# Performance work log

Hardware: AMD Instinct MI355X
Metric: run time of the kernel (lower is better)

The kernel has to match this reference:

```python
import jax, jax.numpy as jnp
import numpy as np

OBS, PRED, NAG, FIN, FOUT, H, NH, FF, NL = 8, 4, 256, 2, 2, 128, 8, 2048, 6


def _lin(x, w, b):
    return x @ w.T + b


def _ln(x, g, b, e=1e-5):
    m = x.mean(-1, keepdims=True)
    v = x.var(-1, keepdims=True)
    return (x - m) / jnp.sqrt(v + e) * g + b


def setup_inputs():
    key = jax.random.key(0)
    ks = iter(jax.random.split(key, 64))

    def w(shape, fan_in):
        return jax.random.normal(next(ks), shape, jnp.float32) / np.float32(np.sqrt(fan_in))

    return dict(
        traj_in=jax.random.normal(next(ks), (OBS + PRED, NAG, FIN), jnp.float32),
        adj_in=jax.random.uniform(next(ks), (OBS, NAG, NAG), jnp.float32),
        eps=jax.random.normal(next(ks), (OBS * NAG, H), jnp.float32),
        pro1_w=w((H, FIN), FIN), pro1_b=jnp.zeros(H, jnp.float32),
        pro2_w=w((H, H), H), pro2_b=jnp.zeros(H, jnp.float32),
        mu_w=w((H, H), H), mu_b=jnp.zeros(H, jnp.float32),
        ls_w=w((H, H), H), ls_b=jnp.zeros(H, jnp.float32),
        gdl_w=w((H, H), H), gdl_b=jnp.zeros(H, jnp.float32),
        pro3_w=w((H, OBS), OBS), pro3_b=jnp.zeros(H, jnp.float32),
        pro4_w=w((OBS, H), H), pro4_b=jnp.zeros(OBS, jnp.float32),
        pro5_w=w((FOUT, H), H), pro5_b=jnp.zeros(FOUT, jnp.float32),
        t_qkv_w=w((NL, 3 * H, H), H), t_qkv_b=jnp.zeros((NL, 3 * H), jnp.float32),
        t_out_w=w((NL, H, H), H), t_out_b=jnp.zeros((NL, H), jnp.float32),
        t_ff1_w=w((NL, FF, H), H), t_ff1_b=jnp.zeros((NL, FF), jnp.float32),
        t_ff2_w=w((NL, H, FF), FF), t_ff2_b=jnp.zeros((NL, H), jnp.float32),
        t_ln1_g=jnp.ones((NL, H), jnp.float32), t_ln1_b=jnp.zeros((NL, H), jnp.float32),
        t_ln2_g=jnp.ones((NL, H), jnp.float32), t_ln2_b=jnp.zeros((NL, H), jnp.float32),
        iftrain=1,
    )


def reference(traj_in, adj_in, eps, pro1_w, pro1_b, pro2_w, pro2_b, mu_w, mu_b,
              ls_w, ls_b, gdl_w, gdl_b, pro3_w, pro3_b, pro4_w, pro4_b,
              pro5_w, pro5_b, t_qkv_w, t_qkv_b, t_out_w, t_out_b,
              t_ff1_w, t_ff1_b, t_ff2_w, t_ff2_b, t_ln1_g, t_ln1_b,
              t_ln2_g, t_ln2_b, iftrain):
    batch_in = traj_in[:OBS, :, :FIN]            # [T, N, Fin]
    tar_y = traj_in[OBS:, :, :FOUT]              # [PRED, N, Fout]

    # block-diagonal adjacency over time, min-max normalized
    A = jax.scipy.linalg.block_diag(*[adj_in[t] for t in range(OBS)])  # [TN, TN]
    ADJ = (A - A.min()) / (A.max() - A.min())

    # GCNConv normalization: add remaining self-loops (weight 1), symmetric D^-1/2 A D^-1/2
    d = jnp.diagonal(ADJ)
    A_sl = ADJ + jnp.diag(jnp.where(d == 0, 1.0, 0.0).astype(ADJ.dtype))
    deg = A_sl.sum(0)
    dis = jnp.where(deg > 0, 1.0 / jnp.sqrt(deg), 0.0)
    agg = (dis[:, None] * A_sl * dis[None, :]).T  # aggregate src(row)->tgt(col)

    enc = _lin(jax.nn.relu(_lin(batch_in, pro1_w, pro1_b)), pro2_w, pro2_b)
    enc = enc.reshape(-1, H)                     # [TN, H]

    # VGAE encode (two GCNConv heads) + reparametrize, PyG clamps logstd at 10
    mu = agg @ _lin(enc, mu_w, mu_b)
    logstd = jnp.minimum(agg @ _lin(enc, ls_w, ls_b), 10.0)
    Z = jnp.where(jnp.asarray(iftrain) > 0, mu + eps * jnp.exp(logstd), mu)
    kld = -0.5 * jnp.mean(jnp.sum(1.0 + 2.0 * logstd - mu ** 2 - jnp.exp(2.0 * logstd), axis=1))

    out = _lin(Z, gdl_w, gdl_b)
    logits = Z @ Z.T                             # [TN, TN]
    struct_loss = jnp.mean(jnp.maximum(logits, 0.0) - logits * ADJ
                           + jnp.log1p(jnp.exp(-jnp.abs(logits))))

    # transformer over agents: [N, H, T] -> pro3 -> [N(seq), H(batch), H(d)]
    x = _lin(out.reshape(OBS, NAG, H).transpose(1, 2, 0), pro3_w, pro3_b)
    dh = H // NH
    S, B = x.shape[0], x.shape[1]
    for l in range(NL):
        qkv = _lin(x, t_qkv_w[l], t_qkv_b[l])
        q, k, v = jnp.split(qkv, 3, axis=-1)
        q = q.reshape(S, B, NH, dh)
        k = k.reshape(S, B, NH, dh)
        v = v.reshape(S, B, NH, dh)
        sc = jnp.einsum('sbhd,tbhd->bhst', q, k) / np.float32(np.sqrt(dh))
        att = jax.nn.softmax(sc, axis=-1)
        o = jnp.einsum('bhst,tbhd->sbhd', att, v).reshape(S, B, H)
        x = _ln(x + _lin(o, t_out_w[l], t_out_b[l]), t_ln1_g[l], t_ln1_b[l])
        f = _lin(jax.nn.relu(_lin(x, t_ff1_w[l], t_ff1_b[l])), t_ff2_w[l], t_ff2_b[l])
        x = _ln(x + f, t_ln2_g[l], t_ln2_b[l])

    out = _lin(x, pro4_w, pro4_b).transpose(2, 0, 1)   # [T, N, H]
    tra = _lin(out, pro5_w, pro5_b)                    # [T, N, Fout]
    traj = tra[-PRED:]
    traj_loss = jnp.sqrt(jnp.sum((traj - tar_y) ** 2, axis=-1)).sum(axis=0).mean()
    loss = traj_loss + kld + struct_loss
    return traj, loss
```

## Files before the change

kernel.cpp:

```cpp
#include <hip/hip_runtime.h>
#include <math.h>


namespace {

constexpr int kOBS = 8, kNAG = 256, kH = 128;
constexpr int kGN = kOBS * kNAG;
constexpr int kROWS = kNAG * kH;

typedef __attribute__((ext_vector_type(8))) short bf16x8;
typedef __attribute__((ext_vector_type(4))) float f32x4;
typedef __attribute__((ext_vector_type(4))) unsigned short us4;

struct Scal {
  int    mn_bits;
  int    mx_bits;
  float  Amin;
  float  invr;
  float  c0;
  int    pad;
  double kld_sum;
  double struct_sum;
  double traj_sum;
};

__device__ inline float waveReduceSum(float v) {
#pragma unroll
  for (int off = 32; off; off >>= 1) v += __shfl_xor(v, off, 64);
  return v;
}

__device__ inline unsigned short f2bf(float f) {
  unsigned u = __float_as_uint(f);
  return (unsigned short)((u + 0x7fffu + ((u >> 16) & 1u)) >> 16);
}
__device__ inline float bf2f(unsigned short h) {
  return __uint_as_float((unsigned)h << 16);
}
__device__ inline void split4(float4 v, us4& h, us4& l) {
  h.x = f2bf(v.x); l.x = f2bf(v.x - bf2f(h.x));
  h.y = f2bf(v.y); l.y = f2bf(v.y - bf2f(h.y));
  h.z = f2bf(v.z); l.z = f2bf(v.z - bf2f(h.z));
  h.w = f2bf(v.w); l.w = f2bf(v.w - bf2f(h.w));
}

__device__ inline int swz4(int c)  { return c ^ ((c >> 3) & 7); }
__device__ inline int swz16(int c) { return c ^ ((c >> 4) & 7); }

#define GLL(g, s)                                             \
  __builtin_amdgcn_global_load_lds(                           \
      (const __attribute__((address_space(1))) void*)(g),     \
      (__attribute__((address_space(3))) void*)(s), 16, 0, 0)

__global__ void k_init(Scal* sc) {
  if (threadIdx.x == 0) {
    sc->mn_bits = 0x7f800000;
    sc->mx_bits = 0xff800000;
    sc->kld_sum = 0.0;
    sc->struct_sum = 0.0;
    sc->traj_sum = 0.0;
  }
}

__global__ void k_minmax(const float* __restrict__ adj, int n, Scal* sc) {
  float lmin = INFINITY, lmax = -INFINITY;
  for (int i = blockIdx.x * blockDim.x + threadIdx.x; i < n;
       i += gridDim.x * blockDim.x) {
    float v = adj[i];
    lmin = fminf(lmin, v);
    lmax = fmaxf(lmax, v);
  }
#pragma unroll
  for (int off = 32; off; off >>= 1) {
    lmin = fminf(lmin, __shfl_xor(lmin, off, 64));
    lmax = fmaxf(lmax, __shfl_xor(lmax, off, 64));
  }
  __shared__ float smn[4], smx[4];
  int w = threadIdx.x >> 6;
  if ((threadIdx.x & 63) == 0) { smn[w] = lmin; smx[w] = lmax; }
  __syncthreads();
  if (threadIdx.x == 0) {
    lmin = fminf(fminf(smn[0], smn[1]), fminf(smn[2], smn[3]));
    lmax = fmaxf(fmaxf(smx[0], smx[1]), fmaxf(smx[2], smx[3]));
    atomicMin(&sc->mn_bits, __float_as_int(lmin));
    atomicMax(&sc->mx_bits, __float_as_int(lmax));
  }
}

__global__ void k_scale(Scal* sc) {
  float mn = fminf(0.0f, __int_as_float(sc->mn_bits));
  float mx = fmaxf(0.0f, __int_as_float(sc->mx_bits));
  sc->Amin = mn;
  sc->invr = 1.0f / (mx - mn);
  sc->c0 = (0.0f - mn) * sc->invr;
}

__global__ void k_dis(const float* __restrict__ adj, const Scal* __restrict__ sc,
                      float* __restrict__ dis) {
  int j = blockIdx.x * 256 + threadIdx.x;
  int t = j >> 8, jj = j & 255;
  const float* a = adj + (size_t)t * 65536;
  float Amin = sc->Amin, invr = sc->invr, c0 = sc->c0;
  float sum = 0.f;
  for (int i = 0; i < 256; ++i) sum += (a[i * 256 + jj] - Amin) * invr;
  float djj = (a[jj * 256 + jj] - Amin) * invr;
  float deg = sum + 1792.0f * c0 + (djj == 0.0f ? 1.0f : 0.0f);
  dis[j] = deg > 0.0f ? 1.0f / sqrtf(deg) : 0.0f;
}

__global__ void k_agg(const float* __restrict__ adj, const Scal* __restrict__ sc,
                      const float* __restrict__ dis, float* __restrict__ agg) {
  int idx = blockIdx.x * 256 + threadIdx.x;
  int t = idx >> 16, i = (idx >> 8) & 255, j = idx & 255;
  float v = (adj[(size_t)t * 65536 + j * 256 + i] - sc->Amin) * sc->invr;
  if (i == j && v == 0.0f) v += 1.0f;
  agg[idx] = dis[t * 256 + j] * v * dis[t * 256 + i];
}

__global__ void k_enc1(const float* __restrict__ traj, const float* __restrict__ w,
                       const float* __restrict__ b, float* __restrict__ out) {
  int idx = blockIdx.x * 256 + threadIdx.x;
  int r = idx >> 7, f = idx & 127;
  float v = traj[r * 2] * w[f * 2] + traj[r * 2 + 1] * w[f * 2 + 1] + b[f];
  out[idx] = fmaxf(v, 0.0f);
}

__global__ void k_cvt(const float* __restrict__ src, unsigned short* __restrict__ h,
                      unsigned short* __restrict__ l, int n4) {
  int i = blockIdx.x * 256 + threadIdx.x;
  if (i >= n4) return;
  float4 v = reinterpret_cast<const float4*>(src)[i];
  us4 hh, ll;
  split4(v, hh, ll);
  reinterpret_cast<us4*>(h)[i] = hh;
  reinterpret_cast<us4*>(l)[i] = ll;
}

#define BM 64
#define BN 64
#define KC 32
#define LP 68

template <bool TB>
__global__ __launch_bounds__(256) void gemm_kernel(
    const float* __restrict__ A, const float* __restrict__ B,
    const float* __restrict__ bias, float* __restrict__ C, int K, int ldb,
    int ldc, int flags, size_t aStride, size_t bStride, size_t cStride) {
  if (blockIdx.z) {
    A += (size_t)blockIdx.z * aStride;
    B += (size_t)blockIdx.z * bStride;
    C += (size_t)blockIdx.z * cStride;
  }
  __shared__ float As[KC][LP];
  __shared__ float Bs[KC][LP];
  const int tid = threadIdx.x;
  const int tx = tid & 15, ty = tid >> 4;
  const int m0 = blockIdx.y * BM, n0 = blockIdx.x * BN;
  float acc[4][4] = {};
  for (int k0 = 0; k0 < K; k0 += KC) {
#pragma unroll
    for (int i = 0; i < 2; ++i) {
      int q = tid + i * 256;
      int row = q >> 3, kq = q & 7;
      float4 v = *reinterpret_cast<const float4*>(
          &A[(size_t)(m0 + row) * K + k0 + kq * 4]);
      As[kq * 4 + 0][row] = v.x;
      As[kq * 4 + 1][row] = v.y;
      As[kq * 4 + 2][row] = v.z;
      As[kq * 4 + 3][row] = v.w;
    }
    if (TB) {
#pragma unroll
      for (int i = 0; i < 2; ++i) {
        int q = tid + i * 256;
        int row = q >> 3, kq = q & 7;
        float4 v = *reinterpret_cast<const float4*>(
            &B[(size_t)(n0 + row) * ldb + k0 + kq * 4]);
        Bs[kq * 4 + 0][row] = v.x;
        Bs[kq * 4 + 1][row] = v.y;
        Bs[kq * 4 + 2][row] = v.z;
        Bs[kq * 4 + 3][row] = v.w;
      }
    } else {
#pragma unroll
      for (int i = 0; i < 2; ++i) {
        int q = tid + i * 256;
        int kr = q >> 4, nq = q & 15;
        float4 v = *reinterpret_cast<const float4*>(
            &B[(size_t)(k0 + kr) * ldb + n0 + nq * 4]);
        *reinterpret_cast<float4*>(&Bs[kr][nq * 4]) = v;
      }
    }
    __syncthreads();
#pragma unroll
    for (int kk = 0; kk < KC; ++kk) {
      float4 a4 = *reinterpret_cast<const float4*>(&As[kk][ty * 4]);
      float4 b4 = *reinterpret_cast<const float4*>(&Bs[kk][tx * 4]);
      float av[4] = {a4.x, a4.y, a4.z, a4.w};
      float bv[4] = {b4.x, b4.y, b4.z, b4.w};
#pragma unroll
      for (int i = 0; i < 4; ++i)
#pragma unroll
        for (int j = 0; j < 4; ++j) acc[i][j] += av[i] * bv[j];
    }
    __syncthreads();
  }
  float bv[4] = {0.f, 0.f, 0.f, 0.f};
  if (bias) {
    float4 b4 = *reinterpret_cast<const float4*>(&bias[n0 + tx * 4]);
    bv[0] = b4.x; bv[1] = b4.y; bv[2] = b4.z; bv[3] = b4.w;
  }
#pragma unroll
  for (int i = 0; i < 4; ++i) {
    float* cp = &C[(size_t)(m0 + ty * 4 + i) * ldc + n0 + tx * 4];
    float4 o;
    float ov[4];
#pragma unroll
    for (int j = 0; j < 4; ++j) ov[j] = acc[i][j] + bv[j];
    if (flags & 2) {
      float4 old = *reinterpret_cast<const float4*>(cp);
      ov[0] += old.x; ov[1] += old.y; ov[2] += old.z; ov[3] += old.w;
    }
    if (flags & 1) {
#pragma unroll
      for (int j = 0; j < 4; ++j) ov[j] = fmaxf(ov[j], 0.0f);
    }
    o.x = ov[0]; o.y = ov[1]; o.z = ov[2]; o.w = ov[3];
    *reinterpret_cast<float4*>(cp) = o;
  }
}

template <int BMb, int BNb>
__global__ __launch_bounds__(256) void gemm_bf(
    const unsigned short* __restrict__ Ah, const unsigned short* __restrict__ Al,
    const unsigned short* __restrict__ Bh, const unsigned short* __restrict__ Bl,
    const float* __restrict__ bias, float* __restrict__ C,
    int K, int lda, int ldb, int ldc, int flags) {
  constexpr int MI = BMb / 32, NI = BNb / 32;
  constexpr int WTM = BMb / 2, WTN = BNb / 2;
  __shared__ unsigned short sAh[BMb * 32], sAl[BMb * 32];
  __shared__ unsigned short sBh[BNb * 32], sBl[BNb * 32];
  const int tid = threadIdx.x, lane = tid & 63, w = tid >> 6;
  const int wr = w >> 1, wc = w & 1;
  const int m0 = blockIdx.y * BMb, n0 = blockIdx.x * BNb;
  f32x4 acc[MI][NI];
#pragma unroll
  for (int i = 0; i < MI; ++i)
#pragma unroll
    for (int j = 0; j < NI; ++j) acc[i][j] = (f32x4){0.f, 0.f, 0.f, 0.f};

  for (int k0 = 0; k0 < K; k0 += 32) {
#pragma unroll
    for (int i = 0; i < BMb / 64; ++i) {
      int c = tid + i * 256;
      int g = swz4(c);
      int row = g >> 2, c4 = g & 3;
      size_t ga = (size_t)(m0 + row) * lda + k0 + c4 * 8;
      GLL(&Ah[ga], &sAh[c * 8]);
      GLL(&Al[ga], &sAl[c * 8]);
    }
#pragma unroll
    for (int i = 0; i < BNb / 64; ++i) {
      int c = tid + i * 256;
      int g = swz4(c);
      int row = g >> 2, c4 = g & 3;
      size_t ga = (size_t)(n0 + row) * ldb + k0 + c4 * 8;
      GLL(&Bh[ga], &sBh[c * 8]);
      GLL(&Bl[ga], &sBl[c * 8]);
    }
    __syncthreads();
    bf16x8 bh[NI], bl[NI];
#pragma unroll
    for (int ni = 0; ni < NI; ++ni) {
      int p = swz4((wc * WTN + ni * 16 + (lane & 15)) * 4 + (lane >> 4));
      bh[ni] = *reinterpret_cast<const bf16x8*>(&sBh[p * 8]);
      bl[ni] = *reinterpret_cast<const bf16x8*>(&sBl[p * 8]);
    }
#pragma unroll
    for (int mi = 0; mi < MI; ++mi) {
      int p = swz4((wr * WTM + mi * 16 + (lane & 15)) * 4 + (lane >> 4));
      bf16x8 ah = *reinterpret_cast<const bf16x8*>(&sAh[p * 8]);
      bf16x8 al = *reinterpret_cast<const bf16x8*>(&sAl[p * 8]);
#pragma unroll
      for (int ni = 0; ni < NI; ++ni) {
        acc[mi][ni] = __builtin_amdgcn_mfma_f32_16x16x32_bf16(
            ah, bh[ni], acc[mi][ni], 0, 0, 0);
        acc[mi][ni] = __builtin_amdgcn_mfma_f32_16x16x32_bf16(
            ah, bl[ni], acc[mi][ni], 0, 0, 0);
        acc[mi][ni] = __builtin_amdgcn_mfma_f32_16x16x32_bf16(
            al, bh[ni], acc[mi][ni], 0, 0, 0);
      }
    }
    __syncthreads();
  }
  const int crow0 = m0 + wr * WTM + (lane >> 4) * 4;
  const int ccol0 = n0 + wc * WTN + (lane & 15);
#pragma unroll
  for (int ni = 0; ni < NI; ++ni) {
    int col = ccol0 + ni * 16;
    float bv = bias ? bias[col] : 0.f;
#pragma unroll
    for (int mi = 0; mi < MI; ++mi) {
#pragma unroll
      for (int r = 0; r < 4; ++r) {
        int row = crow0 + mi * 16 + r;
        float v = acc[mi][ni][r] + bv;
        if (flags & 2) v += C[(size_t)row * ldc + col];
        if (flags & 1) v = fmaxf(v, 0.0f);
        C[(size_t)row * ldc + col] = v;
      }
    }
  }
}

__global__ __launch_bounds__(256) void k_ffn(
    const unsigned short* __restrict__ Xh, const unsigned short* __restrict__ Xl,
    const unsigned short* __restrict__ W1h, const unsigned short* __restrict__ W1l,
    const float* __restrict__ b1,
    const unsigned short* __restrict__ W2h, const unsigned short* __restrict__ W2l,
    const float* __restrict__ b2, float* __restrict__ out) {
  __shared__ unsigned short sLds[40960];
  unsigned short* sPh = sLds + 32768;
  unsigned short* sPl = sLds + 34816;
  float* sB1 = reinterpret_cast<float*>(sLds + 36864);
  const int tid = threadIdx.x, lane = tid & 63, w = tid >> 6;
  const int wr = w >> 1, wc = w & 1;
  const int m0 = blockIdx.x * 64;

  auto stageW = [&](int buf, int f0) {
    unsigned short* d = sLds + buf * 16384;
#pragma unroll
    for (int i = 0; i < 2; ++i) {
      int c = tid + i * 256;
      {
        int g = swz16(c);
        size_t ga = (size_t)(f0 + (g >> 4)) * 128 + (g & 15) * 8;
        GLL(&W1h[ga], &d[c * 8]);
        GLL(&W1l[ga], &d[4096 + c * 8]);
      }
      {
        int g = swz4(c);
        size_t ga = (size_t)(g >> 2) * 2048 + f0 + (g & 3) * 8;
        GLL(&W2h[ga], &d[8192 + c * 8]);
        GLL(&W2l[ga], &d[12288 + c * 8]);
      }
    }
  };

  {
    unsigned short* sXh = sLds + 16384;
    unsigned short* sXl = sLds + 24576;
#pragma unroll
    for (int i = 0; i < 4; ++i) {
      int c = tid + i * 256;
      int g = swz16(c);
      size_t ga = (size_t)(m0 + (g >> 4)) * 128 + (g & 15) * 8;
      GLL(&Xh[ga], &sXh[c * 8]);
      GLL(&Xl[ga], &sXl[c * 8]);
    }
#pragma unroll
    for (int i = 0; i < 2; ++i) {
      int c = tid + i * 256;
      GLL(&b1[c * 4], &sB1[c * 4]);
    }
  }
  __builtin_amdgcn_sched_barrier(0);
  asm volatile("s_waitcnt vmcnt(0)");
  __builtin_amdgcn_sched_barrier(0);
  __builtin_amdgcn_s_barrier();
  stageW(0, 0);
  bf16x8 xah[4][2], xal[4][2];
  {
    unsigned short* sXh = sLds + 16384;
    unsigned short* sXl = sLds + 24576;
#pragma unroll
    for (int ks = 0; ks < 4; ++ks)
#pragma unroll
      for (int mi = 0; mi < 2; ++mi) {
        int row = wr * 32 + mi * 16 + (lane & 15);
        int p = swz16(row * 16 + ks * 4 + (lane >> 4));
        xah[ks][mi] = *reinterpret_cast<const bf16x8*>(&sXh[p * 8]);
        xal[ks][mi] = *reinterpret_cast<const bf16x8*>(&sXl[p * 8]);
      }
  }
  __builtin_amdgcn_sched_barrier(0);
  asm volatile("s_waitcnt lgkmcnt(0)");
  __builtin_amdgcn_sched_barrier(0);
  __builtin_amdgcn_s_barrier();

  f32x4 acc2[2][4];
#pragma unroll
  for (int i = 0; i < 2; ++i)
#pragma unroll
    for (int j = 0; j < 4; ++j) acc2[i][j] = (f32x4){0.f, 0.f, 0.f, 0.f};

  const int pcol = wc * 16 + (lane & 15);

  auto body = [&](int cur, int f0, bool hasNext) {
    unsigned short* bW1h = sLds + cur * 16384;
    unsigned short* bW1l = bW1h + 4096;
    unsigned short* bW2h = bW1h + 8192;
    unsigned short* bW2l = bW1h + 12288;
    if (hasNext) {
      stageW(cur ^ 1, f0 + 32);
      __builtin_amdgcn_sched_barrier(0);
      asm volatile("s_waitcnt vmcnt(8)");
    } else {
      __builtin_amdgcn_sched_barrier(0);
      asm volatile("s_waitcnt vmcnt(0)");
    }
    __builtin_amdgcn_sched_barrier(0);
    __builtin_amdgcn_s_barrier();
    f32x4 acc1[2];
    acc1[0] = (f32x4){0.f, 0.f, 0.f, 0.f};
    acc1[1] = (f32x4){0.f, 0.f, 0.f, 0.f};
#pragma unroll
    for (int ks = 0; ks < 4; ++ks) {
      int p = swz16((wc * 16 + (lane & 15)) * 16 + ks * 4 + (lane >> 4));
      bf16x8 bh = *reinterpret_cast<const bf16x8*>(&bW1h[p * 8]);
      bf16x8 bl = *reinterpret_cast<const bf16x8*>(&bW1l[p * 8]);
#pragma unroll
      for (int mi = 0; mi < 2; ++mi) {
        acc1[mi] = __builtin_amdgcn_mfma_f32_16x16x32_bf16(xah[ks][mi], bh,
                                                           acc1[mi], 0, 0, 0);
        acc1[mi] = __builtin_amdgcn_mfma_f32_16x16x32_bf16(xah[ks][mi], bl,
                                                           acc1[mi], 0, 0, 0);
        acc1[mi] = __builtin_amdgcn_mfma_f32_16x16x32_bf16(xal[ks][mi], bh,
                                                           acc1[mi], 0, 0, 0);
      }
    }
    float b1v = sB1[f0 + pcol];
#pragma unroll
    for (int mi = 0; mi < 2; ++mi)
#pragma unroll
      for (int r = 0; r < 4; ++r) {
        int prow = wr * 32 + mi * 16 + (lane >> 4) * 4 + r;
        float v = fmaxf(acc1[mi][r] + b1v, 0.0f);
        unsigned short h = f2bf(v);
        int p = swz4(prow * 4 + (pcol >> 3));
        sPh[p * 8 + (pcol & 7)] = h;
        sPl[p * 8 + (pcol & 7)] = f2bf(v - bf2f(h));
      }
    __builtin_amdgcn_sched_barrier(0);
    asm volatile("s_waitcnt lgkmcnt(0)");
    __builtin_amdgcn_sched_barrier(0);
    __builtin_amdgcn_s_barrier();
    bf16x8 pah[2], pal[2];
#pragma unroll
    for (int mi = 0; mi < 2; ++mi) {
      int p = swz4((wr * 32 + mi * 16 + (lane & 15)) * 4 + (lane >> 4));
      pah[mi] = *reinterpret_cast<const bf16x8*>(&sPh[p * 8]);
      pal[mi] = *reinterpret_cast<const bf16x8*>(&sPl[p * 8]);
    }
#pragma unroll
    for (int ni = 0; ni < 4; ++ni) {
      int p = swz4((wc * 64 + ni * 16 + (lane & 15)) * 4 + (lane >> 4));
      bf16x8 bh = *reinterpret_cast<const bf16x8*>(&bW2h[p * 8]);
      bf16x8 bl = *reinterpret_cast<const bf16x8*>(&bW2l[p * 8]);
#pragma unroll
      for (int mi = 0; mi < 2; ++mi) {
        acc2[mi][ni] = __builtin_amdgcn_mfma_f32_16x16x32_bf16(
            pah[mi], bh, acc2[mi][ni], 0, 0, 0);
        acc2[mi][ni] = __builtin_amdgcn_mfma_f32_16x16x32_bf16(
            pah[mi], bl, acc2[mi][ni], 0, 0, 0);
        acc2[mi][ni] = __builtin_amdgcn_mfma_f32_16x16x32_bf16(
            pal[mi], bh, acc2[mi][ni], 0, 0, 0);
      }
    }
    __builtin_amdgcn_sched_barrier(0);
    __builtin_amdgcn_s_barrier();
  };

  for (int fc2 = 0; fc2 < 32; ++fc2) {
    body(0, fc2 * 64, true);
    body(1, fc2 * 64 + 32, fc2 != 31);
  }

#pragma unroll
  for (int ni = 0; ni < 4; ++ni) {
    int col = wc * 64 + ni * 16 + (lane & 15);
    float bv = b2[col];
#pragma unroll
    for (int mi = 0; mi < 2; ++mi)
#pragma unroll
      for (int r = 0; r < 4; ++r) {
        int row = m0 + wr * 32 + mi * 16 + (lane >> 4) * 4 + r;
        out[(size_t)row * 128 + col] = acc2[mi][ni][r] + bv;
      }
  }
}

__global__ void k_zkld(const float* __restrict__ mu, const float* __restrict__ lsr,
                       const float* __restrict__ eps, const int* __restrict__ iftrain,
                       float* __restrict__ Z, Scal* sc) {
  int i = blockIdx.x * 256 + threadIdx.x;
  float m = mu[i];
  float ls = fminf(lsr[i], 10.0f);
  float z = (*iftrain > 0) ? m + eps[i] * __expf(ls) : m;
  Z[i] = z;
  float kt = 1.0f + 2.0f * ls - m * m - __expf(2.0f * ls);
  kt = waveReduceSum(kt);
  __shared__ float sh[4];
  int w = threadIdx.x >> 6;
  if ((threadIdx.x & 63) == 0) sh[w] = kt;
  __syncthreads();
  if (threadIdx.x == 0)
    atomicAdd(&sc->kld_sum, (double)(sh[0] + sh[1] + sh[2] + sh[3]));
}

__global__ __launch_bounds__(256) void k_struct(const float* __restrict__ Z,
                                                const float* __restrict__ adj,
                                                Scal* sc) {
  __shared__ float As[KC][LP];
  __shared__ float Bs[KC][LP];
  const int tid = threadIdx.x;
  const int tx = tid & 15, ty = tid >> 4;
  const int m0 = blockIdx.y * BM, n0 = blockIdx.x * BN;
  float acc[4][4] = {};
  for (int k0 = 0; k0 < kH; k0 += KC) {
#pragma unroll
    for (int i = 0; i < 2; ++i) {
      int q = tid + i * 256;
      int row = q >> 3, kq = q & 7;
      float4 va = *reinterpret_cast<const float4*>(
          &Z[(size_t)(m0 + row) * kH + k0 + kq * 4]);
      As[kq * 4 + 0][row] = va.x;
      As[kq * 4 + 1][row] = va.y;
      As[kq * 4 + 2][row] = va.z;
      As[kq * 4 + 3][row] = va.w;
      float4 vb = *reinterpret_cast<const float4*>(
          &Z[(size_t)(n0 + row) * kH + k0 + kq * 4]);
      Bs[kq * 4 + 0][row] = vb.x;
      Bs[kq * 4 + 1][row] = vb.y;
      Bs[kq * 4 + 2][row] = vb.z;
      Bs[kq * 4 + 3][row] = vb.w;
    }
    __syncthreads();
#pragma unroll
    for (int kk = 0; kk < KC; ++kk) {
      float4 a4 = *reinterpret_cast<const float4*>(&As[kk][ty * 4]);
      float4 b4 = *reinterpret_cast<const float4*>(&Bs[kk][tx * 4]);
      float av[4] = {a4.x, a4.y, a4.z, a4.w};
      float bv[4] = {b4.x, b4.y, b4.z, b4.w};
#pragma unroll
      for (int i = 0; i < 4; ++i)
#pragma unroll
        for (int j = 0; j < 4; ++j) acc[i][j] += av[i] * bv[j];
    }
    __syncthreads();
  }
  float Amin = sc->Amin, invr = sc->invr, c0v = sc->c0;
  float lsum = 0.f;
#pragma unroll
  for (int i = 0; i < 4; ++i) {
#pragma unroll
    for (int j = 0; j < 4; ++j) {
      int gi = m0 + ty * 4 + i, gj = n0 + tx * 4 + j;
      float l = acc[i][j];
      float adjv = c0v;
      if ((gi >> 8) == (gj >> 8))
        adjv = (adj[((size_t)(gi >> 8) << 16) + (gi & 255) * 256 + (gj & 255)] -
                Amin) * invr;
      lsum += fmaxf(l, 0.0f) - l * adjv + __logf(1.0f + __expf(-fabsf(l)));
    }
  }
  lsum = waveReduceSum(lsum);
  __shared__ float sh[4];
  int w = threadIdx.x >> 6;
  if ((threadIdx.x & 63) == 0) sh[w] = lsum;
  __syncthreads();
  if (threadIdx.x == 0)
    atomicAdd(&sc->struct_sum, (double)(sh[0] + sh[1] + sh[2] + sh[3]));
}

__global__ void k_x0(const float* __restrict__ gdl, const float* __restrict__ w3,
                     const float* __restrict__ b3, float* __restrict__ X,
                     unsigned short* __restrict__ Xh,
                     unsigned short* __restrict__ Xl) {
  int f = threadIdx.x;
  size_t r = (size_t)blockIdx.x * 2 + threadIdx.y;
  int n = (int)(r >> 7), h = (int)(r & 127);
  float a = b3[f];
#pragma unroll
  for (int o = 0; o < 8; ++o)
    a += gdl[((size_t)o * 256 + n) * 128 + h] * w3[f * 8 + o];
  X[r * 128 + f] = a;
  unsigned short hh = f2bf(a);
  Xh[r * 128 + f] = hh;
  Xl[r * 128 + f] = f2bf(a - bf2f(hh));
}

__global__ __launch_bounds__(256) void k_attn(const float* __restrict__ QKV,
                                              unsigned short* __restrict__ Oh,
                                              unsigned short* __restrict__ Ol) {
  const int head = blockIdx.x, b = blockIdx.y;
  const int s = threadIdx.x;
  __shared__ float ks[256][16];
  __shared__ float vs[256][16];
  const size_t base = ((size_t)s * 128 + b) * 384 + head * 16;
#pragma unroll
  for (int i = 0; i < 4; ++i) {
    *reinterpret_cast<float4*>(&ks[s][i * 4]) =
        *reinterpret_cast<const float4*>(&QKV[base + 128 + i * 4]);
    *reinterpret_cast<float4*>(&vs[s][i * 4]) =
        *reinterpret_cast<const float4*>(&QKV[base + 256 + i * 4]);
  }
  float q[16];
#pragma unroll
  for (int i = 0; i < 4; ++i) {
    float4 v = *reinterpret_cast<const float4*>(&QKV[base + i * 4]);
    q[i * 4 + 0] = v.x * 0.25f; q[i * 4 + 1] = v.y * 0.25f;
    q[i * 4 + 2] = v.z * 0.25f; q[i * 4 + 3] = v.w * 0.25f;
  }
  __syncthreads();
  float m = -1e30f, lsum = 0.f;
  float o[16] = {};
#pragma unroll 2
  for (int t = 0; t < 256; ++t) {
    float kv[16], vv[16];
#pragma unroll
    for (int i = 0; i < 4; ++i) {
      float4 k4 = *reinterpret_cast<const float4*>(&ks[t][i * 4]);
      float4 v4 = *reinterpret_cast<const float4*>(&vs[t][i * 4]);
      kv[i * 4 + 0] = k4.x; kv[i * 4 + 1] = k4.y;
      kv[i * 4 + 2] = k4.z; kv[i * 4 + 3] = k4.w;
      vv[i * 4 + 0] = v4.x; vv[i * 4 + 1] = v4.y;
      vv[i * 4 + 2] = v4.z; vv[i * 4 + 3] = v4.w;
    }
    float d = 0.f;
#pragma unroll
    for (int i = 0; i < 16; ++i) d += q[i] * kv[i];
    if (d > m + 8.f) {
      float c = __expf(m - d);
      lsum *= c;
#pragma unroll
      for (int i = 0; i < 16; ++i) o[i] *= c;
      m = d;
    }
    float p = __expf(d - m);
    lsum += p;
#pragma unroll
    for (int i = 0; i < 16; ++i) o[i] += p * vv[i];
  }
  float inv = 1.0f / lsum;
  size_t ob = ((size_t)s * 128 + b) * 128 + head * 16;
#pragma unroll
  for (int i = 0; i < 4; ++i) {
    float4 v;
    v.x = o[i * 4 + 0] * inv; v.y = o[i * 4 + 1] * inv;
    v.z = o[i * 4 + 2] * inv; v.w = o[i * 4 + 3] * inv;
    us4 hh, ll;
    split4(v, hh, ll);
    *reinterpret_cast<us4*>(&Oh[ob + i * 4]) = hh;
    *reinterpret_cast<us4*>(&Ol[ob + i * 4]) = ll;
  }
}

__global__ __launch_bounds__(256) void k_resid_ln(
    float* __restrict__ X, const float* __restrict__ T,
    const float* __restrict__ g, const float* __restrict__ b,
    unsigned short* __restrict__ Xh, unsigned short* __restrict__ Xl) {
  int lane = threadIdx.x & 63, rl = threadIdx.x >> 6;
  size_t row = (size_t)blockIdx.x * 4 + rl;
  float* xp = X + row * 128;
  const float* tp = T + row * 128;
  float e0 = xp[lane] + tp[lane];
  float e1 = xp[lane + 64] + tp[lane + 64];
  float mean = waveReduceSum(e0 + e1) * 0.0078125f;
  float d0 = e0 - mean, d1 = e1 - mean;
  float var = waveReduceSum(d0 * d0 + d1 * d1) * 0.0078125f;
  float inv = 1.0f / sqrtf(var + 1e-5f);
  float v0 = d0 * inv * g[lane] + b[lane];
  float v1 = d1 * inv * g[lane + 64] + b[lane + 64];
  xp[lane] = v0;
  xp[lane + 64] = v1;
  unsigned short h0 = f2bf(v0), h1 = f2bf(v1);
  Xh[row * 128 + lane] = h0;
  Xl[row * 128 + lane] = f2bf(v0 - bf2f(h0));
  Xh[row * 128 + lane + 64] = h1;
  Xl[row * 128 + lane + 64] = f2bf(v1 - bf2f(h1));
}

__global__ void k_heady(const float* __restrict__ X, const float* __restrict__ w4,
                        const float* __restrict__ b4, float* __restrict__ y) {
  int tid = threadIdx.x;
  int o = tid & 7, rl = tid >> 3;
  size_t r = (size_t)blockIdx.x * 32 + rl;
  const float* xp = X + r * 128;
  const float* wp = w4 + o * 128;
  float a = b4[o];
  for (int f = 0; f < 128; f += 4)
    a += xp[f] * wp[f] + xp[f + 1] * wp[f + 1] + xp[f + 2] * wp[f + 2] +
         xp[f + 3] * wp[f + 3];
  y[r * 8 + o] = a;
}

__global__ void k_traj(const float* __restrict__ y, const float* __restrict__ w5,
                       const float* __restrict__ b5,
                       const float* __restrict__ traj_in, float* __restrict__ dout,
                       Scal* sc) {
  int n = blockIdx.x, lane = threadIdx.x;
  float w0a = w5[lane], w0b = w5[lane + 64];
  float w1a = w5[128 + lane], w1b = w5[128 + lane + 64];
  float dsum = 0.f;
  for (int oi = 0; oi < 4; ++oi) {
    int o = 4 + oi;
    float ya = y[((size_t)n * 128 + lane) * 8 + o];
    float yb = y[((size_t)n * 128 + lane + 64) * 8 + o];
    float s0 = waveReduceSum(w0a * ya + w0b * yb);
    float s1 = waveReduceSum(w1a * ya + w1b * yb);
    if (lane == 0) {
      float t0 = s0 + b5[0], t1 = s1 + b5[1];
      dout[oi * 512 + n * 2 + 0] = t0;
      dout[oi * 512 + n * 2 + 1] = t1;
      float dx = t0 - traj_in[((8 + oi) * 256 + n) * 2 + 0];
      float dy = t1 - traj_in[((8 + oi) * 256 + n) * 2 + 1];
      dsum += sqrtf(dx * dx + dy * dy);
    }
  }
  if (lane == 0) atomicAdd(&sc->traj_sum, (double)dsum);
}

__global__ void k_loss(const Scal* sc, float* dout) {
  if (threadIdx.x == 0) {
    double traj_loss = sc->traj_sum / 256.0;
    double kld = -0.5 * sc->kld_sum / 2048.0;
    double st = sc->struct_sum / (2048.0 * 2048.0);
    dout[2048] = (float)(traj_loss + kld + st);
  }
}

}

extern "C" void kernel_launch(void* const* d_in, const int* in_sizes, int n_in,
                              void* d_out, int out_size, void* d_ws,
                              size_t ws_size, hipStream_t stream) {
  (void)in_sizes; (void)n_in; (void)out_size; (void)ws_size;
  const float* traj_in = (const float*)d_in[0];
  const float* adj     = (const float*)d_in[1];
  const float* eps     = (const float*)d_in[2];
  const float* pro1_w  = (const float*)d_in[3];
  const float* pro1_b  = (const float*)d_in[4];
  const float* pro2_w  = (const float*)d_in[5];
  const float* pro2_b  = (const float*)d_in[6];
  const float* mu_w    = (const float*)d_in[7];
  const float* mu_b    = (const float*)d_in[8];
  const float* ls_w    = (const float*)d_in[9];
  const float* ls_b    = (const float*)d_in[10];
  const float* gdl_w   = (const float*)d_in[11];
  const float* gdl_b   = (const float*)d_in[12];
  const float* pro3_w  = (const float*)d_in[13];
  const float* pro3_b  = (const float*)d_in[14];
  const float* pro4_w  = (const float*)d_in[15];
  const float* pro4_b  = (const float*)d_in[16];
  const float* pro5_w  = (const float*)d_in[17];
  const float* pro5_b  = (const float*)d_in[18];
  const float* qkv_w   = (const float*)d_in[19];
  const float* qkv_b   = (const float*)d_in[20];
  const float* outp_w  = (const float*)d_in[21];
  const float* outp_b  = (const float*)d_in[22];
  const float* ff1_w   = (const float*)d_in[23];
  const float* ff1_b   = (const float*)d_in[24];
  const float* ff2_w   = (const float*)d_in[25];
  const float* ff2_b   = (const float*)d_in[26];
  const float* ln1_g   = (const float*)d_in[27];
  const float* ln1_b   = (const float*)d_in[28];
  const float* ln2_g   = (const float*)d_in[29];
  const float* ln2_b   = (const float*)d_in[30];
  const int*   iftrain = (const int*)d_in[31];
  float* dout = (float*)d_out;

  char* wsb = (char*)d_ws;
  size_t off = 0;
  auto alloc = [&](size_t bytes) {
    char* p = wsb + off;
    off += (bytes + 255) & ~(size_t)255;
    return p;
  };
  Scal* sc    = (Scal*)alloc(256);
  float* dis  = (float*)alloc(kGN * 4);
  float* agg  = (float*)alloc((size_t)kOBS * 65536 * 4);
  float* enc1 = (float*)alloc((size_t)kGN * kH * 4);
  float* enc  = (float*)alloc((size_t)kGN * kH * 4);
  float* Mmu  = (float*)alloc((size_t)kGN * kH * 4);
  float* Mls  = (float*)alloc((size_t)kGN * kH * 4);
  float* mu   = (float*)alloc((size_t)kGN * kH * 4);
  float* lsb  = (float*)alloc((size_t)kGN * kH * 4);
  float* Z    = (float*)alloc((size_t)kGN * kH * 4);
  float* gdl  = (float*)alloc((size_t)kGN * kH * 4);
  float* X    = (float*)alloc((size_t)kROWS * kH * 4);
  unsigned short* Xh = (unsigned short*)alloc((size_t)kROWS * kH * 2);
  unsigned short* Xl = (unsigned short*)alloc((size_t)kROWS * kH * 2);
  float* QKV = (float*)alloc((size_t)kROWS * 384 * 4);
  unsigned short* Oh = (unsigned short*)alloc((size_t)kROWS * kH * 2);
  unsigned short* Ol = (unsigned short*)alloc((size_t)kROWS * kH * 2);
  float* tmp  = (float*)alloc((size_t)kROWS * kH * 4);
  float* y    = (float*)alloc((size_t)kROWS * 8 * 4);
  unsigned short* qkvWh = (unsigned short*)alloc(6 * 384 * 128 * 2);
  unsigned short* qkvWl = (unsigned short*)alloc(6 * 384 * 128 * 2);
  unsigned short* outWh = (unsigned short*)alloc(6 * 128 * 128 * 2);
  unsigned short* outWl = (unsigned short*)alloc(6 * 128 * 128 * 2);
  unsigned short* ff1Wh = (unsigned short*)alloc(6 * 2048 * 128 * 2);
  unsigned short* ff1Wl = (unsigned short*)alloc(6 * 2048 * 128 * 2);
  unsigned short* ff2Wh = (unsigned short*)alloc(6 * 128 * 2048 * 2);
  unsigned short* ff2Wl = (unsigned short*)alloc(6 * 128 * 2048 * 2);

  auto gemm_nt_small = [&](const float* A, const float* B, const float* bias,
                           float* C, int M, int N, int K, int ldb, int ldc,
                           int flags) {
    dim3 g(N / 64, M / 64, 1);
    gemm_kernel<true><<<g, 256, 0, stream>>>(A, B, bias, C, K, ldb, ldc, flags,
                                             (size_t)0, (size_t)0, (size_t)0);
  };

  k_cvt<<<(6 * 384 * 128 / 4 + 255) / 256, 256, 0, stream>>>(
      qkv_w, qkvWh, qkvWl, 6 * 384 * 128 / 4);
  k_cvt<<<(6 * 128 * 128 / 4 + 255) / 256, 256, 0, stream>>>(
      outp_w, outWh, outWl, 6 * 128 * 128 / 4);
  k_cvt<<<(6 * 2048 * 128 / 4 + 255) / 256, 256, 0, stream>>>(
      ff1_w, ff1Wh, ff1Wl, 6 * 2048 * 128 / 4);
  k_cvt<<<(6 * 128 * 2048 / 4 + 255) / 256, 256, 0, stream>>>(
      ff2_w, ff2Wh, ff2Wl, 6 * 128 * 2048 / 4);

  k_init<<<1, 64, 0, stream>>>(sc);
  k_minmax<<<512, 256, 0, stream>>>(adj, kOBS * kNAG * kNAG, sc);
  k_scale<<<1, 1, 0, stream>>>(sc);
  k_dis<<<8, 256, 0, stream>>>(adj, sc, dis);
  k_agg<<<2048, 256, 0, stream>>>(adj, sc, dis, agg);

  k_enc1<<<(kGN * kH) / 256, 256, 0, stream>>>(traj_in, pro1_w, pro1_b, enc1);
  gemm_nt_small(enc1, pro2_w, pro2_b, enc, kGN, kH, kH, kH, kH, 0);
  gemm_nt_small(enc, mu_w, mu_b, Mmu, kGN, kH, kH, kH, kH, 0);
  gemm_nt_small(enc, ls_w, ls_b, Mls, kGN, kH, kH, kH, kH, 0);
  {
    dim3 g(kH / 64, kNAG / 64, kOBS);
    gemm_kernel<false><<<g, 256, 0, stream>>>(agg, Mmu, nullptr, mu, kNAG, kH,
                                              kH, 0, (size_t)65536,
                                              (size_t)kNAG * kH, (size_t)kNAG * kH);
    gemm_kernel<false><<<g, 256, 0, stream>>>(agg, Mls, nullptr, lsb, kNAG, kH,
                                              kH, 0, (size_t)65536,
                                              (size_t)kNAG * kH, (size_t)kNAG * kH);
  }
  k_zkld<<<(kGN * kH) / 256, 256, 0, stream>>>(mu, lsb, eps, iftrain, Z, sc);
  gemm_nt_small(Z, gdl_w, gdl_b, gdl, kGN, kH, kH, kH, kH, 0);
  k_struct<<<dim3(kGN / 64, kGN / 64), 256, 0, stream>>>(Z, adj, sc);
  k_x0<<<kROWS / 2, dim3(128, 2), 0, stream>>>(gdl, pro3_w, pro3_b, X, Xh, Xl);

  for (int l = 0; l < 6; ++l) {
    gemm_bf<128, 128><<<dim3(3, kROWS / 128), 256, 0, stream>>>(
        Xh, Xl, qkvWh + (size_t)l * 384 * 128, qkvWl + (size_t)l * 384 * 128,
        qkv_b + l * 384, QKV, 128, 128, 128, 384, 0);
    k_attn<<<dim3(8, 128), 256, 0, stream>>>(QKV, Oh, Ol);
    gemm_bf<64, 128><<<dim3(1, kROWS / 64), 256, 0, stream>>>(
        Oh, Ol, outWh + (size_t)l * 128 * 128, outWl + (size_t)l * 128 * 128,
        outp_b + l * 128, tmp, 128, 128, 128, 128, 0);
    k_resid_ln<<<kROWS / 4, 256, 0, stream>>>(X, tmp, ln1_g + l * kH,
                                              ln1_b + l * kH, Xh, Xl);
    k_ffn<<<kROWS / 64, 256, 0, stream>>>(
        Xh, Xl, ff1Wh + (size_t)l * 2048 * 128, ff1Wl + (size_t)l * 2048 * 128,
        ff1_b + l * 2048, ff2Wh + (size_t)l * 128 * 2048,
        ff2Wl + (size_t)l * 128 * 2048, ff2_b + l * 128, tmp);
    k_resid_ln<<<kROWS / 4, 256, 0, stream>>>(X, tmp, ln2_g + l * kH,
                                              ln2_b + l * kH, Xh, Xl);
  }

  k_heady<<<kROWS / 32, 256, 0, stream>>>(X, pro4_w, pro4_b, y);
  k_traj<<<kNAG, 64, 0, stream>>>(y, pro5_w, pro5_b, traj_in, dout, sc);
  k_loss<<<1, 1, 0, stream>>>(sc, dout);
}
```

Baseline: 1.913 ms.

## Rewrite attention kernel to use bf16 split-precision MFMA with online softmax

Replaces the scalar per-thread attention loop with an MFMA-based flash-style kernel. Q, K and V are split into bf16 hi/lo pairs in shared memory, with V stored transposed. QK^T and PV are computed with three-term split MFMAs (hi*hi, hi*lo, lo*hi) to approximate fp32 accuracy, with a running max and sum per 32-key block. The goal is to cut the ALU-bound scalar dot products. The cost is extra conversion work, half-empty MFMA operands because head dim 16 is padded to 32, and a small loss of precision.

Result: faster. 1.651 ms (-13.7%).

```diff
diff --git a/kernel.cpp b/kernel.cpp
--- a/kernel.cpp
+++ b/kernel.cpp
@@ -9,6 +9,7 @@
 constexpr int kROWS = kNAG * kH;
 
 typedef __attribute__((ext_vector_type(8))) short bf16x8;
+typedef __attribute__((ext_vector_type(4))) short s16x4;
 typedef __attribute__((ext_vector_type(4))) float f32x4;
 typedef __attribute__((ext_vector_type(4))) unsigned short us4;
 
@@ -42,6 +43,13 @@
   h.y = f2bf(v.y); l.y = f2bf(v.y - bf2f(h.y));
   h.z = f2bf(v.z); l.z = f2bf(v.z - bf2f(h.z));
   h.w = f2bf(v.w); l.w = f2bf(v.w - bf2f(h.w));
+}
+
+__device__ inline bf16x8 ld_bf8(const unsigned short* p) {
+  union { bf16x8 v; s16x4 h[2]; } u;
+  u.h[0] = *reinterpret_cast<const s16x4*>(p);
+  u.h[1] = *reinterpret_cast<const s16x4*>(p + 4);
+  return u.v;
 }
 
 __device__ inline int swz4(int c)  { return c ^ ((c >> 3) & 7); }
@@ -593,66 +601,128 @@
 __global__ __launch_bounds__(256) void k_attn(const float* __restrict__ QKV,
                                               unsigned short* __restrict__ Oh,
                                               unsigned short* __restrict__ Ol) {
+  __shared__ unsigned short sQh[256 * 20], sQl[256 * 20];
+  __shared__ unsigned short sKh[256 * 20], sKl[256 * 20];
+  __shared__ unsigned short sVh[16 * 264], sVl[16 * 264];
   const int head = blockIdx.x, b = blockIdx.y;
-  const int s = threadIdx.x;
-  __shared__ float ks[256][16];
-  __shared__ float vs[256][16];
-  const size_t base = ((size_t)s * 128 + b) * 384 + head * 16;
-#pragma unroll
-  for (int i = 0; i < 4; ++i) {
-    *reinterpret_cast<float4*>(&ks[s][i * 4]) =
-        *reinterpret_cast<const float4*>(&QKV[base + 128 + i * 4]);
-    *reinterpret_cast<float4*>(&vs[s][i * 4]) =
-        *reinterpret_cast<const float4*>(&QKV[base + 256 + i * 4]);
-  }
-  float q[16];
-#pragma unroll
-  for (int i = 0; i < 4; ++i) {
-    float4 v = *reinterpret_cast<const float4*>(&QKV[base + i * 4]);
-    q[i * 4 + 0] = v.x * 0.25f; q[i * 4 + 1] = v.y * 0.25f;
-    q[i * 4 + 2] = v.z * 0.25f; q[i * 4 + 3] = v.w * 0.25f;
+  const int tid = threadIdx.x;
+  const int lane = tid & 63, w = tid >> 6;
+  const int g = lane >> 4, x = lane & 15;
+
+  {
+    const size_t base = ((size_t)tid * 128 + b) * 384 + (size_t)head * 16;
+#pragma unroll
+    for (int j = 0; j < 4; ++j) {
+      float4 qv = *reinterpret_cast<const float4*>(&QKV[base + j * 4]);
+      qv.x *= 0.25f; qv.y *= 0.25f; qv.z *= 0.25f; qv.w *= 0.25f;
+      us4 h, l;
+      split4(qv, h, l);
+      *reinterpret_cast<us4*>(&sQh[tid * 20 + j * 4]) = h;
+      *reinterpret_cast<us4*>(&sQl[tid * 20 + j * 4]) = l;
+      float4 kv = *reinterpret_cast<const float4*>(&QKV[base + 128 + j * 4]);
+      split4(kv, h, l);
+      *reinterpret_cast<us4*>(&sKh[tid * 20 + j * 4]) = h;
+      *reinterpret_cast<us4*>(&sKl[tid * 20 + j * 4]) = l;
+      float4 vv = *reinterpret_cast<const float4*>(&QKV[base + 256 + j * 4]);
+      split4(vv, h, l);
+      sVh[(j * 4 + 0) * 264 + tid] = h.x; sVl[(j * 4 + 0) * 264 + tid] = l.x;
+      sVh[(j * 4 + 1) * 264 + tid] = h.y; sVl[(j * 4 + 1) * 264 + tid] = l.y;
+      sVh[(j * 4 + 2) * 264 + tid] = h.z; sVl[(j * 4 + 2) * 264 + tid] = l.z;
+      sVh[(j * 4 + 3) * 264 + tid] = h.w; sVl[(j * 4 + 3) * 264 + tid] = l.w;
+    }
   }
   __syncthreads();
-  float m = -1e30f, lsum = 0.f;
-  float o[16] = {};
-#pragma unroll 2
-  for (int t = 0; t < 256; ++t) {
-    float kv[16], vv[16];
-#pragma unroll
-    for (int i = 0; i < 4; ++i) {
-      float4 k4 = *reinterpret_cast<const float4*>(&ks[t][i * 4]);
-      float4 v4 = *reinterpret_cast<const float4*>(&vs[t][i * 4]);
-      kv[i * 4 + 0] = k4.x; kv[i * 4 + 1] = k4.y;
-      kv[i * 4 + 2] = k4.z; kv[i * 4 + 3] = k4.w;
-      vv[i * 4 + 0] = v4.x; vv[i * 4 + 1] = v4.y;
-      vv[i * 4 + 2] = v4.z; vv[i * 4 + 3] = v4.w;
-    }
-    float d = 0.f;
-#pragma unroll
-    for (int i = 0; i < 16; ++i) d += q[i] * kv[i];
-    if (d > m + 8.f) {
-      float c = __expf(m - d);
-      lsum *= c;
-#pragma unroll
-      for (int i = 0; i < 16; ++i) o[i] *= c;
-      m = d;
-    }
-    float p = __expf(d - m);
-    lsum += p;
-#pragma unroll
-    for (int i = 0; i < 16; ++i) o[i] += p * vv[i];
-  }
-  float inv = 1.0f / lsum;
-  size_t ob = ((size_t)s * 128 + b) * 128 + head * 16;
-#pragma unroll
-  for (int i = 0; i < 4; ++i) {
-    float4 v;
-    v.x = o[i * 4 + 0] * inv; v.y = o[i * 4 + 1] * inv;
-    v.z = o[i * 4 + 2] * inv; v.w = o[i * 4 + 3] * inv;
-    us4 hh, ll;
-    split4(v, hh, ll);
-    *reinterpret_cast<us4*>(&Oh[ob + i * 4]) = hh;
-    *reinterpret_cast<us4*>(&Ol[ob + i * 4]) = ll;
+
+  const bf16x8 zero8 = {0, 0, 0, 0, 0, 0, 0, 0};
+  bf16x8 qbh[4], qbl[4];
+#pragma unroll
+  for (int qi = 0; qi < 4; ++qi) {
+    if (g < 2) {
+      int row = w * 64 + qi * 16 + x;
+      qbh[qi] = ld_bf8(&sQh[row * 20 + 8 * g]);
+      qbl[qi] = ld_bf8(&sQl[row * 20 + 8 * g]);
+    } else {
+      qbh[qi] = zero8;
+      qbl[qi] = zero8;
+    }
+  }
+
+  f32x4 oacc[4];
+  float mrun[4], lrun[4];
+#pragma unroll
+  for (int qi = 0; qi < 4; ++qi) {
+    oacc[qi] = (f32x4){0.f, 0.f, 0.f, 0.f};
+    mrun[qi] = -1e30f;
+    lrun[qi] = 0.f;
+  }
+
+  for (int b32 = 0; b32 < 8; ++b32) {
+    const int xa = 32 * b32 + 8 * (x >> 2) + (x & 3);
+    const int xb = xa + 4;
+    bf16x8 kah = zero8, kal = zero8, kbh = zero8, kbl = zero8;
+    if (g < 2) {
+      kah = ld_bf8(&sKh[xa * 20 + 8 * g]);
+      kal = ld_bf8(&sKl[xa * 20 + 8 * g]);
+      kbh = ld_bf8(&sKh[xb * 20 + 8 * g]);
+      kbl = ld_bf8(&sKl[xb * 20 + 8 * g]);
+    }
+    const bf16x8 vth = ld_bf8(&sVh[x * 264 + 32 * b32 + 8 * g]);
+    const bf16x8 vtl = ld_bf8(&sVl[x * 264 + 32 * b32 + 8 * g]);
+#pragma unroll
+    for (int qi = 0; qi < 4; ++qi) {
+      f32x4 sA = (f32x4){0.f, 0.f, 0.f, 0.f};
+      f32x4 sB = (f32x4){0.f, 0.f, 0.f, 0.f};
+      sA = __builtin_amdgcn_mfma_f32_16x16x32_bf16(kah, qbh[qi], sA, 0, 0, 0);
+      sA = __builtin_amdgcn_mfma_f32_16x16x32_bf16(kah, qbl[qi], sA, 0, 0, 0);
+      sA = __builtin_amdgcn_mfma_f32_16x16x32_bf16(kal, qbh[qi], sA, 0, 0, 0);
+      sB = __builtin_amdgcn_mfma_f32_16x16x32_bf16(kbh, qbh[qi], sB, 0, 0, 0);
+      sB = __builtin_amdgcn_mfma_f32_16x16x32_bf16(kbh, qbl[qi], sB, 0, 0, 0);
+      sB = __builtin_amdgcn_mfma_f32_16x16x32_bf16(kbl, qbh[qi], sB, 0, 0, 0);
+      float mt = fmaxf(fmaxf(fmaxf(sA[0], sA[1]), fmaxf(sA[2], sA[3])),
+                       fmaxf(fmaxf(sB[0], sB[1]), fmaxf(sB[2], sB[3])));
+      mt = fmaxf(mt, __shfl_xor(mt, 16));
+      mt = fmaxf(mt, __shfl_xor(mt, 32));
+      const float mnew = fmaxf(mrun[qi], mt);
+      const float c = __expf(mrun[qi] - mnew);
+      mrun[qi] = mnew;
+      float p[8];
+      p[0] = __expf(sA[0] - mnew); p[1] = __expf(sA[1] - mnew);
+      p[2] = __expf(sA[2] - mnew); p[3] = __expf(sA[3] - mnew);
+      p[4] = __expf(sB[0] - mnew); p[5] = __expf(sB[1] - mnew);
+      p[6] = __expf(sB[2] - mnew); p[7] = __expf(sB[3] - mnew);
+      lrun[qi] = lrun[qi] * c +
+                 ((p[0] + p[1]) + (p[2] + p[3])) +
+                 ((p[4] + p[5]) + (p[6] + p[7]));
+      union { bf16x8 v; unsigned short s[8]; } ph, pl;
+#pragma unroll
+      for (int i = 0; i < 8; ++i) {
+        unsigned short h = f2bf(p[i]);
+        ph.s[i] = h;
+        pl.s[i] = f2bf(p[i] - bf2f(h));
+      }
+      f32x4 o = oacc[qi] * c;
+      o = __builtin_amdgcn_mfma_f32_16x16x32_bf16(vth, ph.v, o, 0, 0, 0);
+      o = __builtin_amdgcn_mfma_f32_16x16x32_bf16(vth, pl.v, o, 0, 0, 0);
+      o = __builtin_amdgcn_mfma_f32_16x16x32_bf16(vtl, ph.v, o, 0, 0, 0);
+      oacc[qi] = o;
+    }
+  }
+
+#pragma unroll
+  for (int qi = 0; qi < 4; ++qi) {
+    float lt = lrun[qi];
+    lt += __shfl_xor(lt, 16);
+    lt += __shfl_xor(lt, 32);
+    const float inv = 1.0f / lt;
+    const int qrow = w * 64 + qi * 16 + x;
+    const size_t ob = ((size_t)qrow * 128 + b) * 128 + head * 16 + 4 * g;
+    float4 ov;
+    ov.x = oacc[qi][0] * inv; ov.y = oacc[qi][1] * inv;
+    ov.z = oacc[qi][2] * inv; ov.w = oacc[qi][3] * inv;
+    us4 h, l;
+    split4(ov, h, l);
+    *reinterpret_cast<us4*>(&Oh[ob]) = h;
+    *reinterpret_cast<us4*>(&Ol[ob]) = l;
   }
 }
 
```
